# Kernel tuning notes

Measured on AMD Instinct MI355X. Metric: run time of the kernel, lower is better.

The kernel has to match this reference:

```python
import jax, jax.numpy as jnp
import numpy as np

B, SQ, SKV, D, H = 2, 2048, 2048, 1024, 16
HD = D // H

def setup_inputs() -> dict:
    key = jax.random.key(0)
    ks = jax.random.split(key, 11)
    def xavier(k, shape):
        fan_in, fan_out = shape[1], shape[0]
        lim = jnp.sqrt(6.0 / (fan_in + fan_out))
        return jax.random.uniform(k, shape, jnp.float32, -lim, lim)
    return {
        'query': jax.random.normal(ks[0], (B, SQ, D), jnp.float32),
        'key': jax.random.normal(ks[1], (B, SKV, D), jnp.float32),
        'value': jax.random.normal(ks[2], (B, SKV, D), jnp.float32),
        'Wq': xavier(ks[3], (D, D)), 'bq': jnp.zeros((D,), jnp.float32),
        'Wk': xavier(ks[4], (D, D)), 'bk': jnp.zeros((D,), jnp.float32),
        'Wv': xavier(ks[5], (D, D)), 'bv': jnp.zeros((D,), jnp.float32),
        'Wo': xavier(ks[6], (D, D)), 'bo': jnp.zeros((D,), jnp.float32),
    }

def reference(query, key, value, Wq, bq, Wk, bk, Wv, bv, Wo, bo):
    # Linear uses y = x @ W.T + b (torch convention, W: [out, in])
    Q = query @ Wq.T + bq   # [B, SQ, D]
    K = key @ Wk.T + bk     # [B, SKV, D]
    V = value @ Wv.T + bv   # [B, SKV, D]
    Q = Q.reshape(B, SQ, H, HD).transpose(0, 2, 1, 3)   # [B,H,SQ,HD]
    K = K.reshape(B, SKV, H, HD).transpose(0, 2, 1, 3)  # [B,H,SKV,HD]
    V = V.reshape(B, SKV, H, HD).transpose(0, 2, 1, 3)
    scores = jnp.einsum('bhqd,bhkd->bhqk', Q, K) / jnp.sqrt(jnp.float32(HD))
    probs = jax.nn.softmax(scores, axis=-1)  # dropout is identity at eval
    ctx = jnp.einsum('bhqk,bhkd->bhqd', probs, V)
    ctx = ctx.transpose(0, 2, 1, 3).reshape(B, SQ, D)
    return ctx @ Wo.T + bo
```

## Files before the change

kernel.cpp:

```cpp
#include <hip/hip_runtime.h>

#define DIM   1024
#define NHEAD 16
#define HDIM  64
#define BATCH 2
#define SEQ   2048
#define MTOT  4096

typedef unsigned short u16;
typedef unsigned int   u32;
typedef __attribute__((ext_vector_type(8))) short bf16x8;
typedef __attribute__((ext_vector_type(4))) float f32x4;
typedef __attribute__((ext_vector_type(4))) u32   u32x4;

#define QSCALE 0.18033688011112042f
#define EXP2F(x) __builtin_amdgcn_exp2f(x)
#define SWAP32(a, b) asm volatile("v_permlane32_swap_b32 %0, %1" : "+v"(a), "+v"(b))
#define SWAP16(a, b) asm volatile("v_permlane16_swap_b32 %0, %1" : "+v"(a), "+v"(b))

__device__ __forceinline__ void gload_lds16(const void* g, void* l) {
  __builtin_amdgcn_global_load_lds((const __attribute__((address_space(1))) void*)g,
                                   (__attribute__((address_space(3))) void*)l, 16, 0, 0);
}

__device__ __forceinline__ u16 f32_to_bf16(float f) {
  union { float f; u32 u; } v; v.f = f;
  u32 r = v.u + 0x7fffu + ((v.u >> 16) & 1u);
  return (u16)(r >> 16);
}

__device__ __forceinline__ u32 pack_bf16(float a, float b) {
  return (u32)f32_to_bf16(a) | ((u32)f32_to_bf16(b) << 16);
}

struct CvtArgs {
  const float* s[7];
  u16*         d[7];
  int          n8[7];
};

__global__ __launch_bounds__(256) void cvt_all(CvtArgs a) {
  const int z = blockIdx.z;
  const float* s = a.s[z];
  u16* d = a.d[z];
  const int n8 = a.n8[z];
  const int stride = gridDim.x * blockDim.x;
  for (int i = blockIdx.x * blockDim.x + threadIdx.x; i < n8; i += stride) {
    float4 x = ((const float4*)s)[2 * i], y = ((const float4*)s)[2 * i + 1];
    u32x4 o;
    o[0] = pack_bf16(x.x, x.y); o[1] = pack_bf16(x.z, x.w);
    o[2] = pack_bf16(y.x, y.y); o[3] = pack_bf16(y.z, y.w);
    *(u32x4*)&d[(size_t)i * 8] = o;
  }
}

template<int MF, bool OUTF32, bool BIAS_ROW>
__device__ __forceinline__ void gemm_body(
    const u16* __restrict__ X, const u16* __restrict__ W,
    const float* __restrict__ bias, void* __restrict__ Cv, int ldc, float scale,
    int m0, int n0)
{
  __shared__ __align__(16) u16 ldsA[32 * 4 * 64];
  __shared__ __align__(16) u16 ldsB[128 * 64];
  const int tid  = threadIdx.x;
  const int lane = tid & 63;
  const int wid  = tid >> 6;
  const int wr   = wid >> 1, wc = wid & 1;
  const int srow = tid >> 3;
  const int scs  = tid & 7;

  f32x4 acc[MF][4];
#pragma unroll
  for (int mf = 0; mf < MF; ++mf)
#pragma unroll
    for (int nf = 0; nf < 4; ++nf)
#pragma unroll
      for (int r = 0; r < 4; ++r) acc[mf][nf][r] = 0.f;

  for (int kt = 0; kt < DIM; kt += 64) {
    __syncthreads();
#pragma unroll
    for (int call = 0; call < MF; ++call) {
      int row = call * 32 + srow;
      int lc  = scs ^ (row & 7);
      gload_lds16(X + (size_t)(m0 + row) * DIM + kt + lc * 8,
                  &ldsA[(row * 8 + scs) * 8]);
    }
#pragma unroll
    for (int call = 0; call < 4; ++call) {
      int row = call * 32 + srow;
      int lc  = scs ^ (row & 7);
      gload_lds16(W + (size_t)(n0 + row) * DIM + kt + lc * 8,
                  &ldsB[(row * 8 + scs) * 8]);
    }
    __syncthreads();
#pragma unroll
    for (int ks = 0; ks < 2; ++ks) {
      bf16x8 af[MF], bfr[4];
#pragma unroll
      for (int mf = 0; mf < MF; ++mf) {
        int row = wr * (16 * MF) + mf * 16 + (lane & 15);
        int ch  = (ks * 4 + (lane >> 4)) ^ (row & 7);
        af[mf] = *(const bf16x8*)&ldsA[row * 64 + ch * 8];
      }
#pragma unroll
      for (int nf = 0; nf < 4; ++nf) {
        int row = wc * 64 + nf * 16 + (lane & 15);
        int ch  = (ks * 4 + (lane >> 4)) ^ (row & 7);
        bfr[nf] = *(const bf16x8*)&ldsB[row * 64 + ch * 8];
      }
#pragma unroll
      for (int mf = 0; mf < MF; ++mf)
#pragma unroll
        for (int nf = 0; nf < 4; ++nf)
          acc[mf][nf] = __builtin_amdgcn_mfma_f32_16x16x32_bf16(
              af[mf], bfr[nf], acc[mf][nf], 0, 0, 0);
    }
  }
#pragma unroll
  for (int nf = 0; nf < 4; ++nf) {
    int col = n0 + wc * 64 + nf * 16 + (lane & 15);
    float bcol = BIAS_ROW ? 0.f : bias[col];
#pragma unroll
    for (int mf = 0; mf < MF; ++mf) {
      int rbase = m0 + wr * (16 * MF) + mf * 16 + ((lane >> 4) << 2);
#pragma unroll
      for (int r = 0; r < 4; ++r) {
        float bv = BIAS_ROW ? bias[rbase + r] : bcol;
        float v = (acc[mf][nf][r] + bv) * scale;
        if (OUTF32) ((float*)Cv)[(size_t)(rbase + r) * ldc + col] = v;
        else        ((u16*)Cv)[(size_t)(rbase + r) * ldc + col] = f32_to_bf16(v);
      }
    }
  }
}

__global__ __launch_bounds__(256, 2) void gemm_proj_kernel(
    const u16* __restrict__ q, const u16* __restrict__ k, const u16* __restrict__ v,
    const u16* __restrict__ wq, const u16* __restrict__ wk, const u16* __restrict__ wv,
    const float* __restrict__ bq, const float* __restrict__ bk, const float* __restrict__ bv,
    u16* __restrict__ oq, u16* __restrict__ ok, u16* __restrict__ ovt)
{
  const int bid = blockIdx.x;
  const int wk_ = (bid & 7) * 96 + (bid >> 3);
  const int z = wk_ >> 8, rem = wk_ & 255;
  const int ty = rem >> 3, tx = rem & 7;
  if (z == 0)
    gemm_body<4, false, false>(q, wq, bq, oq, DIM, QSCALE, ty * 128, tx * 128);
  else if (z == 1)
    gemm_body<4, false, false>(k, wk, bk, ok, DIM, 1.0f, ty * 128, tx * 128);
  else
    gemm_body<4, false, true>(wv, v, bv, ovt, MTOT, 1.0f, tx * 128, ty * 128);
}

__global__ __launch_bounds__(256, 2) void gemm_o_kernel(
    const u16* __restrict__ x, const u16* __restrict__ w,
    const float* __restrict__ b, float* __restrict__ c)
{
  const int bid = blockIdx.x;
  const int wk_ = (bid & 7) * 64 + (bid >> 3);
  const int ty = wk_ >> 3, tx = wk_ & 7;
  gemm_body<2, true, false>(x, w, b, c, DIM, 1.0f, ty * 64, tx * 128);
}

__global__ __launch_bounds__(256, 3) void attn_kernel(
    const u16* __restrict__ Qm, const u16* __restrict__ Km,
    const u16* __restrict__ Vt, u16* __restrict__ Cm)
{
  __shared__ __align__(16) u16 Kl[2][64 * 64];
  __shared__ __align__(16) u16 Vl[2][64 * 64];

  const int tid = threadIdx.x, lane = tid & 63, wid = tid >> 6;
  const int c = lane & 15, g = lane >> 4;
  const int wkid = (blockIdx.x & 7) * 64 + (blockIdx.x >> 3);
  const int qt = wkid & 15;
  const int bh = wkid >> 4;
  const int b = bh >> 4, h = bh & 15;
  const size_t hb = (size_t)h * HDIM;
  const int q0 = qt * 128 + wid * 32;
  const u16* Qh = Qm + ((size_t)b * SEQ + q0) * DIM + hb;
  const u16* Kh = Km + (size_t)b * SEQ * DIM + hb;
  const u16* Vh = Vt + (size_t)(h * HDIM) * MTOT + (size_t)b * SEQ;

  bf16x8 qf[2][2];
#pragma unroll
  for (int mf = 0; mf < 2; ++mf)
#pragma unroll
    for (int ks = 0; ks < 2; ++ks)
      qf[mf][ks] = *(const bf16x8*)(Qh + (size_t)(16 * mf + c) * DIM + ks * 32 + g * 8);

  bf16x8 ones;
#pragma unroll
  for (int j = 0; j < 8; ++j) ((short*)&ones)[j] = (short)0x3F80;

  f32x4 oacc[2][4], lacc[2];
#pragma unroll
  for (int mf = 0; mf < 2; ++mf) {
#pragma unroll
    for (int nd = 0; nd < 4; ++nd)
#pragma unroll
      for (int r = 0; r < 4; ++r) oacc[mf][nd][r] = 0.f;
#pragma unroll
    for (int r = 0; r < 4; ++r) lacc[mf][r] = 0.f;
  }

  const int srow = tid >> 3, scs = tid & 7;

#define STAGE(T, BUF)                                                          \
  {                                                                            \
    const int kvs = (T) * 64;                                                  \
    _Pragma("unroll")                                                          \
    for (int call = 0; call < 2; ++call) {                                     \
      int row = call * 32 + srow;                                              \
      int lc  = scs ^ (row & 7);                                               \
      gload_lds16(Kh + (size_t)(kvs + row) * DIM + lc * 8,                     \
                  &Kl[BUF][(row * 8 + scs) * 8]);                              \
      gload_lds16(Vh + (size_t)row * MTOT + kvs + lc * 8,                      \
                  &Vl[BUF][(row * 8 + scs) * 8]);                              \
    }                                                                          \
  }

  STAGE(0, 0);

  for (int t = 0; t < 32; ++t) {
    const int cur = t & 1;
    if (t < 31) {
      STAGE(t + 1, cur ^ 1);
      asm volatile("s_waitcnt vmcnt(4)" ::: "memory");
    } else {
      asm volatile("s_waitcnt vmcnt(0)" ::: "memory");
    }
    __builtin_amdgcn_sched_barrier(0);
    __builtin_amdgcn_s_barrier();
    __builtin_amdgcn_sched_barrier(0);

    f32x4 sacc[4][2];
#pragma unroll
    for (int nvk = 0; nvk < 4; ++nvk)
#pragma unroll
      for (int mf = 0; mf < 2; ++mf)
#pragma unroll
        for (int r = 0; r < 4; ++r) sacc[nvk][mf][r] = 0.f;
#pragma unroll
    for (int ks = 0; ks < 2; ++ks) {
      bf16x8 kf[4];
#pragma unroll
      for (int nvk = 0; nvk < 4; ++nvk) {
        int row = nvk * 16 + c;
        int ch  = (ks * 4 + g) ^ (row & 7);
        kf[nvk] = *(const bf16x8*)&Kl[cur][row * 64 + ch * 8];
      }
#pragma unroll
      for (int nvk = 0; nvk < 4; ++nvk)
#pragma unroll
        for (int mf = 0; mf < 2; ++mf)
          sacc[nvk][mf] = __builtin_amdgcn_mfma_f32_16x16x32_bf16(
              kf[nvk], qf[mf][ks], sacc[nvk][mf], 0, 0, 0);
    }

    u32 W[4][2][2];
#pragma unroll
    for (int nvk = 0; nvk < 4; ++nvk)
#pragma unroll
      for (int mf = 0; mf < 2; ++mf) {
        W[nvk][mf][0] = pack_bf16(EXP2F(sacc[nvk][mf][0]), EXP2F(sacc[nvk][mf][1]));
        W[nvk][mf][1] = pack_bf16(EXP2F(sacc[nvk][mf][2]), EXP2F(sacc[nvk][mf][3]));
      }

#pragma unroll
    for (int ks = 0; ks < 2; ++ks) {
      bf16x8 vfr[4];
#pragma unroll
      for (int nd = 0; nd < 4; ++nd) {
        int row = nd * 16 + c;
        int ch  = (ks * 4 + g) ^ (row & 7);
        vfr[nd] = *(const bf16x8*)&Vl[cur][row * 64 + ch * 8];
      }
#pragma unroll
      for (int mf = 0; mf < 2; ++mf) {
        u32 a0 = W[2 * ks][mf][0], b0 = W[2 * ks + 1][mf][0];
        u32 a1 = W[2 * ks][mf][1], b1 = W[2 * ks + 1][mf][1];
        SWAP32(a0, b0); SWAP16(a0, b0);
        SWAP32(a1, b1); SWAP16(a1, b1);
        u32x4 pw4; pw4[0] = a0; pw4[1] = a1; pw4[2] = b0; pw4[3] = b1;
        bf16x8 pa = __builtin_bit_cast(bf16x8, pw4);
        lacc[mf] = __builtin_amdgcn_mfma_f32_16x16x32_bf16(
            pa, ones, lacc[mf], 0, 0, 0);
#pragma unroll
        for (int nd = 0; nd < 4; ++nd)
          oacc[mf][nd] = __builtin_amdgcn_mfma_f32_16x16x32_bf16(
              pa, vfr[nd], oacc[mf][nd], 0, 0, 0);
      }
    }

    __builtin_amdgcn_sched_barrier(0);
    __builtin_amdgcn_s_barrier();
  }
#undef STAGE

#pragma unroll
  for (int mf = 0; mf < 2; ++mf)
#pragma unroll
    for (int nd = 0; nd < 4; ++nd)
#pragma unroll
      for (int r = 0; r < 4; ++r) {
        int q = q0 + 16 * mf + 4 * g + r;
        float v = oacc[mf][nd][r] / lacc[mf][r];
        Cm[((size_t)b * SEQ + q) * DIM + hb + nd * 16 + c] = f32_to_bf16(v);
      }
}

extern "C" void kernel_launch(void* const* d_in, const int* in_sizes, int n_in,
                              void* d_out, int out_size, void* d_ws, size_t ws_size,
                              hipStream_t stream)
{
  const float* query = (const float*)d_in[0];
  const float* key   = (const float*)d_in[1];
  const float* value = (const float*)d_in[2];
  const float* Wq = (const float*)d_in[3];  const float* bq = (const float*)d_in[4];
  const float* Wk = (const float*)d_in[5];  const float* bk = (const float*)d_in[6];
  const float* Wv = (const float*)d_in[7];  const float* bv = (const float*)d_in[8];
  const float* Wo = (const float*)d_in[9];  const float* bo = (const float*)d_in[10];
  float* out = (float*)d_out;

  const size_t NQKV = (size_t)MTOT * DIM;
  const size_t NW   = (size_t)DIM * DIM;
  u16* base = (u16*)d_ws;
  u16* Qb  = base;
  u16* Kb  = Qb + NQKV;
  u16* Vtb = Kb + NQKV;
  u16* Cb  = Vtb + NQKV;
  u16* qc  = Cb + NQKV;
  u16* kc  = qc + NQKV;
  u16* vc  = kc + NQKV;
  u16* wqc = vc + NQKV;
  u16* wkc = wqc + NW;
  u16* wvc = wkc + NW;
  u16* woc = wvc + NW;

  CvtArgs ca;
  ca.s[0] = query; ca.s[1] = key; ca.s[2] = value;
  ca.s[3] = Wq; ca.s[4] = Wk; ca.s[5] = Wv; ca.s[6] = Wo;
  ca.d[0] = qc; ca.d[1] = kc; ca.d[2] = vc;
  ca.d[3] = wqc; ca.d[4] = wkc; ca.d[5] = wvc; ca.d[6] = woc;
  for (int i = 0; i < 3; ++i) ca.n8[i] = (int)(NQKV / 8);
  for (int i = 3; i < 7; ++i) ca.n8[i] = (int)(NW / 8);
  cvt_all<<<dim3(256, 1, 7), 256, 0, stream>>>(ca);

  dim3 blk(256);
  gemm_proj_kernel<<<768, blk, 0, stream>>>(
      qc, kc, vc, wqc, wkc, wvc, bq, bk, bv, Qb, Kb, Vtb);
  attn_kernel<<<512, blk, 0, stream>>>(Qb, Kb, Vtb, Cb);
  gemm_o_kernel<<<512, blk, 0, stream>>>(Cb, woc, bo, out);
}
```

Measured before the change: 125.6 us.

## Double KV tile to 128 keys per iteration and raise wave priority during MFMA

The attention loop now stages 128 keys of K and V per iteration instead of 64, halving the number of barrier-synchronised iterations. The V tile uses a 16-chunk XOR swizzle, and the QK loop is restructured per key block so exp2 runs right after each block's scores. s_setprio brackets the compute section. LDS use doubles and launch bounds drop from 3 to 2 blocks per CU, trading occupancy for fewer barriers and deeper tiles.

After: 120.9 us. -3.7%, faster.

```diff
diff --git a/kernel.cpp b/kernel.cpp
--- a/kernel.cpp
+++ b/kernel.cpp
@@ -163,12 +163,12 @@
   gemm_body<2, true, false>(x, w, b, c, DIM, 1.0f, ty * 64, tx * 128);
 }
 
-__global__ __launch_bounds__(256, 3) void attn_kernel(
+__global__ __launch_bounds__(256, 2) void attn_kernel(
     const u16* __restrict__ Qm, const u16* __restrict__ Km,
     const u16* __restrict__ Vt, u16* __restrict__ Cm)
 {
-  __shared__ __align__(16) u16 Kl[2][64 * 64];
-  __shared__ __align__(16) u16 Vl[2][64 * 64];
+  __shared__ __align__(16) u16 Kl[2][128 * 64];
+  __shared__ __align__(16) u16 Vl[2][64 * 128];
 
   const int tid = threadIdx.x, lane = tid & 63, wid = tid >> 6;
   const int c = lane & 15, g = lane >> 4;
@@ -205,76 +205,75 @@
   }
 
   const int srow = tid >> 3, scs = tid & 7;
+  const int srow2 = tid >> 4, scs2 = tid & 15;
 
 #define STAGE(T, BUF)                                                          \
   {                                                                            \
-    const int kvs = (T) * 64;                                                  \
+    const int kvs = (T) * 128;                                                 \
     _Pragma("unroll")                                                          \
-    for (int call = 0; call < 2; ++call) {                                     \
+    for (int call = 0; call < 4; ++call) {                                     \
       int row = call * 32 + srow;                                              \
       int lc  = scs ^ (row & 7);                                               \
       gload_lds16(Kh + (size_t)(kvs + row) * DIM + lc * 8,                     \
                   &Kl[BUF][(row * 8 + scs) * 8]);                              \
+    }                                                                          \
+    _Pragma("unroll")                                                          \
+    for (int call = 0; call < 4; ++call) {                                     \
+      int row = call * 16 + srow2;                                             \
+      int lc  = scs2 ^ (row & 15);                                             \
       gload_lds16(Vh + (size_t)row * MTOT + kvs + lc * 8,                      \
-                  &Vl[BUF][(row * 8 + scs) * 8]);                              \
+                  &Vl[BUF][(row * 16 + scs2) * 8]);                            \
     }                                                                          \
   }
 
   STAGE(0, 0);
 
-  for (int t = 0; t < 32; ++t) {
+  for (int t = 0; t < 16; ++t) {
     const int cur = t & 1;
-    if (t < 31) {
+    if (t < 15) {
       STAGE(t + 1, cur ^ 1);
-      asm volatile("s_waitcnt vmcnt(4)" ::: "memory");
+      asm volatile("s_waitcnt vmcnt(8)" ::: "memory");
     } else {
       asm volatile("s_waitcnt vmcnt(0)" ::: "memory");
     }
     __builtin_amdgcn_sched_barrier(0);
     __builtin_amdgcn_s_barrier();
     __builtin_amdgcn_sched_barrier(0);
-
-    f32x4 sacc[4][2];
-#pragma unroll
-    for (int nvk = 0; nvk < 4; ++nvk)
+    __builtin_amdgcn_s_setprio(1);
+
+    u32 W[8][2][2];
+#pragma unroll
+    for (int nvk = 0; nvk < 8; ++nvk) {
+      int row = nvk * 16 + c;
+      f32x4 sacc[2];
 #pragma unroll
       for (int mf = 0; mf < 2; ++mf)
 #pragma unroll
-        for (int r = 0; r < 4; ++r) sacc[nvk][mf][r] = 0.f;
-#pragma unroll
-    for (int ks = 0; ks < 2; ++ks) {
-      bf16x8 kf[4];
-#pragma unroll
-      for (int nvk = 0; nvk < 4; ++nvk) {
-        int row = nvk * 16 + c;
-        int ch  = (ks * 4 + g) ^ (row & 7);
-        kf[nvk] = *(const bf16x8*)&Kl[cur][row * 64 + ch * 8];
-      }
-#pragma unroll
-      for (int nvk = 0; nvk < 4; ++nvk)
+        for (int r = 0; r < 4; ++r) sacc[mf][r] = 0.f;
+#pragma unroll
+      for (int ks = 0; ks < 2; ++ks) {
+        int ch = (ks * 4 + g) ^ (row & 7);
+        bf16x8 kf = *(const bf16x8*)&Kl[cur][row * 64 + ch * 8];
 #pragma unroll
         for (int mf = 0; mf < 2; ++mf)
-          sacc[nvk][mf] = __builtin_amdgcn_mfma_f32_16x16x32_bf16(
-              kf[nvk], qf[mf][ks], sacc[nvk][mf], 0, 0, 0);
-    }
-
-    u32 W[4][2][2];
-#pragma unroll
-    for (int nvk = 0; nvk < 4; ++nvk)
+          sacc[mf] = __builtin_amdgcn_mfma_f32_16x16x32_bf16(
+              kf, qf[mf][ks], sacc[mf], 0, 0, 0);
+      }
 #pragma unroll
       for (int mf = 0; mf < 2; ++mf) {
-        W[nvk][mf][0] = pack_bf16(EXP2F(sacc[nvk][mf][0]), EXP2F(sacc[nvk][mf][1]));
-        W[nvk][mf][1] = pack_bf16(EXP2F(sacc[nvk][mf][2]), EXP2F(sacc[nvk][mf][3]));
-      }
-
-#pragma unroll
-    for (int ks = 0; ks < 2; ++ks) {
+        W[nvk][mf][0] = pack_bf16(EXP2F(sacc[mf][0]), EXP2F(sacc[mf][1]));
+        W[nvk][mf][1] = pack_bf16(EXP2F(sacc[mf][2]), EXP2F(sacc[mf][3]));
+      }
+    }
+
+#pragma unroll
+    for (int ks = 0; ks < 4; ++ks) {
       bf16x8 vfr[4];
 #pragma unroll
       for (int nd = 0; nd < 4; ++nd) {
         int row = nd * 16 + c;
-        int ch  = (ks * 4 + g) ^ (row & 7);
-        vfr[nd] = *(const bf16x8*)&Vl[cur][row * 64 + ch * 8];
+        int ch  = (ks * 4 + g) ^ (row & 15);
+        vfr[nd] = *(const bf16x8*)&Vl[cur][row * 128 + ch * 8];
       }
 #pragma unroll
       for (int mf = 0; mf < 2; ++mf) {
@@ -293,6 +292,7 @@
       }
     }
 
+    __builtin_amdgcn_s_setprio(0);
     __builtin_amdgcn_sched_barrier(0);
     __builtin_amdgcn_s_barrier();
   }
```

## Split attention KV range in two halves and add a combine kernel

Applied to the files above, without the earlier changes.

The attention grid doubles: each block now handles half of the KV sequence, so 1024 blocks run instead of 512, and launch bounds rise to 4 blocks per CU. Each block writes unnormalized partial outputs in bf16 and its partial row sums into reused workspace. A new combine kernel adds the two partials and divides by the total sum. This targets underfilled CUs in the attention stage, at the cost of an extra kernel launch, extra memory traffic, and bf16 rounding of the partial outputs. It also raises wave priority with s_setprio around the MFMA section.

Measured after the change: 123.5 us. No clear change (-1.6%).

```diff
diff --git a/kernel.cpp b/kernel.cpp
--- a/kernel.cpp
+++ b/kernel.cpp
@@ -27,6 +27,10 @@
   union { float f; u32 u; } v; v.f = f;
   u32 r = v.u + 0x7fffu + ((v.u >> 16) & 1u);
   return (u16)(r >> 16);
+}
+
+__device__ __forceinline__ float bf16_to_f32(u16 u) {
+  union { u32 u; float f; } v; v.u = ((u32)u) << 16; return v.f;
 }
 
 __device__ __forceinline__ u32 pack_bf16(float a, float b) {
@@ -163,24 +167,28 @@
   gemm_body<2, true, false>(x, w, b, c, DIM, 1.0f, ty * 64, tx * 128);
 }
 
-__global__ __launch_bounds__(256, 3) void attn_kernel(
+__global__ __launch_bounds__(256, 4) void attn_kernel(
     const u16* __restrict__ Qm, const u16* __restrict__ Km,
-    const u16* __restrict__ Vt, u16* __restrict__ Cm)
+    const u16* __restrict__ Vt, u16* __restrict__ PoB, float* __restrict__ LpB)
 {
   __shared__ __align__(16) u16 Kl[2][64 * 64];
   __shared__ __align__(16) u16 Vl[2][64 * 64];
 
   const int tid = threadIdx.x, lane = tid & 63, wid = tid >> 6;
   const int c = lane & 15, g = lane >> 4;
-  const int wkid = (blockIdx.x & 7) * 64 + (blockIdx.x >> 3);
-  const int qt = wkid & 15;
-  const int bh = wkid >> 4;
+  const int wkid = (blockIdx.x & 7) * 128 + (blockIdx.x >> 3);
+  const int half = wkid & 1;
+  const int qt = (wkid >> 1) & 15;
+  const int bh = wkid >> 5;
   const int b = bh >> 4, h = bh & 15;
   const size_t hb = (size_t)h * HDIM;
   const int q0 = qt * 128 + wid * 32;
+  const int kvbase = half * (SEQ / 2);
   const u16* Qh = Qm + ((size_t)b * SEQ + q0) * DIM + hb;
   const u16* Kh = Km + (size_t)b * SEQ * DIM + hb;
   const u16* Vh = Vt + (size_t)(h * HDIM) * MTOT + (size_t)b * SEQ;
+  u16*  Po = PoB + (size_t)half * MTOT * DIM;
+  float* Lp = LpB + (size_t)half * MTOT * NHEAD;
 
   bf16x8 qf[2][2];
 #pragma unroll
@@ -208,7 +216,7 @@
 
 #define STAGE(T, BUF)                                                          \
   {                                                                            \
-    const int kvs = (T) * 64;                                                  \
+    const int kvs = kvbase + (T) * 64;                                         \
     _Pragma("unroll")                                                          \
     for (int call = 0; call < 2; ++call) {                                     \
       int row = call * 32 + srow;                                              \
@@ -222,9 +230,9 @@
 
   STAGE(0, 0);
 
-  for (int t = 0; t < 32; ++t) {
+  for (int t = 0; t < 16; ++t) {
     const int cur = t & 1;
-    if (t < 31) {
+    if (t < 15) {
       STAGE(t + 1, cur ^ 1);
       asm volatile("s_waitcnt vmcnt(4)" ::: "memory");
     } else {
@@ -233,6 +241,7 @@
     __builtin_amdgcn_sched_barrier(0);
     __builtin_amdgcn_s_barrier();
     __builtin_amdgcn_sched_barrier(0);
+    __builtin_amdgcn_s_setprio(1);
 
     f32x4 sacc[4][2];
 #pragma unroll
@@ -293,21 +302,59 @@
       }
     }
 
+    __builtin_amdgcn_s_setprio(0);
     __builtin_amdgcn_sched_barrier(0);
     __builtin_amdgcn_s_barrier();
   }
 #undef STAGE
 
 #pragma unroll
-  for (int mf = 0; mf < 2; ++mf)
+  for (int mf = 0; mf < 2; ++mf) {
 #pragma unroll
     for (int nd = 0; nd < 4; ++nd)
 #pragma unroll
       for (int r = 0; r < 4; ++r) {
         int q = q0 + 16 * mf + 4 * g + r;
-        float v = oacc[mf][nd][r] / lacc[mf][r];
-        Cm[((size_t)b * SEQ + q) * DIM + hb + nd * 16 + c] = f32_to_bf16(v);
-      }
+        Po[((size_t)b * SEQ + q) * DIM + hb + nd * 16 + c] =
+            f32_to_bf16(oacc[mf][nd][r]);
+      }
+    if (c == 0) {
+#pragma unroll
+      for (int r = 0; r < 4; ++r) {
+        int q = q0 + 16 * mf + 4 * g + r;
+        Lp[((size_t)b * SEQ + q) * NHEAD + h] = lacc[mf][r];
+      }
+    }
+  }
+}
+
+__global__ __launch_bounds__(256) void combine_kernel(
+    const u16* __restrict__ P0, const u16* __restrict__ P1,
+    const float* __restrict__ LpB, u16* __restrict__ Cb)
+{
+  const int n8 = (int)((size_t)MTOT * DIM / 8);
+  const int stride = gridDim.x * blockDim.x;
+  const float* L0 = LpB;
+  const float* L1 = LpB + (size_t)MTOT * NHEAD;
+  for (int i = blockIdx.x * blockDim.x + threadIdx.x; i < n8; i += stride) {
+    size_t base = (size_t)i * 8;
+    int qg = (int)(base >> 10);
+    int h  = ((int)(base & 1023)) >> 6;
+    float l = L0[(size_t)qg * NHEAD + h] + L1[(size_t)qg * NHEAD + h];
+    float rl = 1.0f / l;
+    u32x4 a = *(const u32x4*)&P0[base];
+    u32x4 bb = *(const u32x4*)&P1[base];
+    u32x4 o;
+#pragma unroll
+    for (int j = 0; j < 4; ++j) {
+      float lo = (bf16_to_f32((u16)(a[j] & 0xFFFF)) +
+                  bf16_to_f32((u16)(bb[j] & 0xFFFF))) * rl;
+      float hi = (bf16_to_f32((u16)(a[j] >> 16)) +
+                  bf16_to_f32((u16)(bb[j] >> 16))) * rl;
+      o[j] = pack_bf16(lo, hi);
+    }
+    *(u32x4*)&Cb[base] = o;
+  }
 }
 
 extern "C" void kernel_launch(void* const* d_in, const int* in_sizes, int n_in,
@@ -350,6 +397,7 @@
   dim3 blk(256);
   gemm_proj_kernel<<<768, blk, 0, stream>>>(
       qc, kc, vc, wqc, wkc, wvc, bq, bk, bv, Qb, Kb, Vtb);
-  attn_kernel<<<512, blk, 0, stream>>>(Qb, Kb, Vtb, Cb);
+  attn_kernel<<<1024, blk, 0, stream>>>(Qb, Kb, Vtb, qc, (float*)vc);
+  combine_kernel<<<1024, blk, 0, stream>>>(qc, kc, (const float*)vc, Cb);
   gemm_o_kernel<<<512, blk, 0, stream>>>(Cb, woc, bo, out);
 }
```
